# Performance work log

Measured on AMD Instinct MI355X. Metric: run time of the kernel, lower is better.

The kernel has to match this reference:

```python
import jax, jax.numpy as jnp
import numpy as np

B, N, T, D, H, K = 8, 100, 16, 4, 64, 2
E = N * (N - 1)  # 9900 directed edges (fully connected, no self-loops)


def setup_inputs() -> dict:
    key = jax.random.key(0)
    ks = jax.random.split(key, 12)
    inputs = jax.random.normal(ks[0], (B, N, T, D), jnp.float32)
    # edge-type distribution per directed pair (softmax over K types)
    rel_type = jax.nn.softmax(jax.random.normal(ks[1], (B, E, K), jnp.float32), axis=-1)
    # one-hot receiver / sender incidence matrices for fully-connected graph
    off = ~np.eye(N, dtype=bool)
    send_idx, rec_idx = np.where(off)
    eye = np.eye(N, dtype=np.float32)
    rel_rec = jnp.asarray(eye[rec_idx])    # [E, N]
    rel_send = jnp.asarray(eye[send_idx])  # [E, N]
    s = 0.1
    msg_fc1_w = jax.random.normal(ks[2], (K, H, 2 * D), jnp.float32) * s
    msg_fc1_b = jax.random.normal(ks[3], (K, H), jnp.float32) * s
    msg_fc2_w = jax.random.normal(ks[4], (K, H, H), jnp.float32) * s
    msg_fc2_b = jax.random.normal(ks[5], (K, H), jnp.float32) * s
    out_fc1_w = jax.random.normal(ks[6], (H, D + H), jnp.float32) * s
    out_fc1_b = jax.random.normal(ks[7], (H,), jnp.float32) * s
    out_fc2_w = jax.random.normal(ks[8], (H, H), jnp.float32) * s
    out_fc2_b = jax.random.normal(ks[9], (H,), jnp.float32) * s
    out_fc3_w = jax.random.normal(ks[10], (D, H), jnp.float32) * s
    out_fc3_b = jax.random.normal(ks[11], (D,), jnp.float32) * s
    return {
        "inputs": inputs, "rel_type": rel_type,
        "rel_rec": rel_rec, "rel_send": rel_send,
        "msg_fc1_w": msg_fc1_w, "msg_fc1_b": msg_fc1_b,
        "msg_fc2_w": msg_fc2_w, "msg_fc2_b": msg_fc2_b,
        "out_fc1_w": out_fc1_w, "out_fc1_b": out_fc1_b,
        "out_fc2_w": out_fc2_w, "out_fc2_b": out_fc2_b,
        "out_fc3_w": out_fc3_w, "out_fc3_b": out_fc3_b,
        "pred_steps": 1,
    }


def reference(inputs, rel_type, rel_rec, rel_send,
              msg_fc1_w, msg_fc1_b, msg_fc2_w, msg_fc2_b,
              out_fc1_w, out_fc1_b, out_fc2_w, out_fc2_b,
              out_fc3_w, out_fc3_b, pred_steps):
    # inputs: [B, N, T, D] -> [B, T, N, D]
    x = jnp.transpose(inputs, (0, 2, 1, 3))
    b, t, n, d = x.shape
    # rel_type: [B, E, K] -> [B, T, E, K]
    rt = jnp.broadcast_to(rel_type[:, None], (b, t, rel_type.shape[1], rel_type.shape[2]))

    def single_step(xs, rts):
        # gather endpoint states: [B, T', E, D]
        recv = jnp.einsum('en,btnd->bted', rel_rec, xs)
        send = jnp.einsum('en,btnd->bted', rel_send, xs)
        pre_msg = jnp.concatenate([send, recv], axis=-1)  # [B, T', E, 2D]
        # per-edge-type MLP, skipping edge type 0 (skip_first_edge_type=True)
        h1 = jax.nn.relu(jnp.einsum('btef,khf->btekh', pre_msg, msg_fc1_w[1:]) + msg_fc1_b[1:])
        h2 = jax.nn.relu(jnp.einsum('btekh,kgh->btekg', h1, msg_fc2_w[1:]) + msg_fc2_b[1:])
        # mask by edge-type weight and sum over types -> [B, T', E, H]
        all_msgs = jnp.einsum('btekh,btek->bteh', h2, rts[..., 1:])
        # aggregate messages at receivers: [B, T', N, H]
        agg = jnp.einsum('bteh,en->btnh', all_msgs, rel_rec)
        aug = jnp.concatenate([xs, agg], axis=-1)  # [B, T', N, D+H]
        p = jax.nn.relu(aug @ out_fc1_w.T + out_fc1_b)
        p = jax.nn.relu(p @ out_fc2_w.T + out_fc2_b)
        p = p @ out_fc3_w.T + out_fc3_b
        return xs + p

    last_pred = x[:, 0::pred_steps]
    curr_rt = rt[:, 0::pred_steps]
    preds = []
    for _ in range(pred_steps):
        last_pred = single_step(last_pred, curr_rt)
        preds.append(last_pred)
    tp = preds[0].shape[1]
    # interleave: output[:, i::pred_steps] = preds[i]
    output = jnp.stack(preds, axis=2).reshape(b, tp * pred_steps, n, d)
    pred_all = output[:, : t - 1]  # [B, T-1, N, D]
    return jnp.transpose(pred_all, (0, 2, 1, 3))  # [B, N, T-1, D]
```

## Files before the change

### kernel.cpp

```cpp
#include <hip/hip_runtime.h>
#include <hip/hip_fp16.h>

#define B_  8
#define N_  100
#define T_  16
#define TP_ 15
#define D_  4
#define H_  64
#define E_  9900
#define NG  25
#define ROWS 12000

#define WS_AIN 0u
#define WS_V   2304000u
#define WS_RTT 3840000u
#define WS_UBF 4198400u
#define WS_W2F 5928960u
#define WS_W1F 5937152u
#define WS_W2B 5949440u
#define WS_W3F 5957632u

typedef __attribute__((ext_vector_type(8))) _Float16 f16x8;
typedef __attribute__((ext_vector_type(4))) float f32x4;

__device__ __forceinline__ void gload_lds16(const void* g, void* lds) {
    __builtin_amdgcn_global_load_lds(
        (const __attribute__((address_space(1))) void*)g,
        (__attribute__((address_space(3))) void*)lds, 16, 0, 0);
}

__device__ __forceinline__ f16x8 relu_add8(uint4 u, uint4 v) {
    const f16x8 a = __builtin_bit_cast(f16x8, u);
    const f16x8 b = __builtin_bit_cast(f16x8, v);
    const f16x8 s = a + b;
    const f16x8 z = (f16x8)(_Float16)0;
    return __builtin_elementwise_max(s, z);
}

__global__ __launch_bounds__(256)
void nri_prep(const float* __restrict__ x, const float* __restrict__ rel,
              const float* __restrict__ w1, const float* __restrict__ b1,
              const float* __restrict__ w2, const float* __restrict__ f1w,
              const float* __restrict__ f2w, const float* __restrict__ f3w,
              __half* __restrict__ ubf, __half* __restrict__ v_h,
              float* __restrict__ rtt, __half* __restrict__ ain,
              __half* __restrict__ w2f, __half* __restrict__ w1f,
              __half* __restrict__ w2b, __half* __restrict__ w3f)
{
    const int lane = threadIdx.x & 63;
    const int wid  = blockIdx.x * 4 + (threadIdx.x >> 6);

    if (wid < ROWS) {
        const int nn = wid % N_;
        const int bt = wid / N_;
        const int t  = bt % TP_;
        const int b  = bt / TP_;
        const float4 ws4 = *(const float4*)(w1 + lane * 8);
        const float4 wr4 = *(const float4*)(w1 + lane * 8 + 4);
        const float4 xv  = *(const float4*)(x + (((size_t)b * N_ + nn) * T_ + t) * D_);
        const float u = ws4.x * xv.x + ws4.y * xv.y + ws4.z * xv.z + ws4.w * xv.w;
        const float v = wr4.x * xv.x + wr4.y * xv.y + wr4.z * xv.z + wr4.w * xv.w
                        + b1[lane];
        ubf[(size_t)bt * 7200 + nn * 72 + lane] = __float2half(u);
        v_h[(size_t)wid * 64 + lane] = __float2half(v);
        if (lane == 32) {
            const unsigned short h0 = __half_as_ushort(__float2half(xv.x));
            const unsigned short h1 = __half_as_ushort(__float2half(xv.y));
            const unsigned short h2 = __half_as_ushort(__float2half(xv.z));
            const unsigned short h3 = __half_as_ushort(__float2half(xv.w));
            uint2 p; p.x = (unsigned)h0 | ((unsigned)h1 << 16);
                     p.y = (unsigned)h2 | ((unsigned)h3 << 16);
            *(uint2*)(ain + (size_t)wid * 96 + 64) = p;
        } else if (lane >= 33 && lane < 40) {
            uint2 zz; zz.x = 0u; zz.y = 0u;
            *(uint2*)(ain + (size_t)wid * 96 + 68 + (lane - 33) * 4) = zz;
        }
    } else if (wid < ROWS + B_ * N_) {
        const int idx = wid - ROWS;
        const int n = idx % N_;
        const int b = idx / N_;
        float* dst = rtt + (size_t)idx * 112;
        const int ia  = lane + (lane >= n ? 1 : 0);
        const int eda = ia * (N_ - 1) + (n < ia ? n : n - 1);
        dst[lane] = rel[((size_t)b * E_ + eda) * 2 + 1];
        if (lane < 48) {
            const int e2 = 64 + lane;
            float rv = 0.f;
            if (e2 < N_ - 1) {
                const int ib  = e2 + (e2 >= n ? 1 : 0);
                const int edb = ib * (N_ - 1) + (n < ib ? n : n - 1);
                rv = rel[((size_t)b * E_ + edb) * 2 + 1];
            }
            dst[64 + lane] = rv;
        }
    } else {
        const int fid = wid - (ROWS + B_ * N_);
        const int g16 = lane & 15, q = lane >> 4;
        unsigned short h[8];
        if (fid < 8) {
            const int s = fid >> 2, nt = fid & 3;
            const int g = nt * 16 + g16;
            #pragma unroll
            for (int j = 0; j < 8; ++j)
                h[j] = __half_as_ushort(__float2half(
                    w2[(size_t)g * 64 + s * 32 + q * 8 + j]));
            uint4 pv; pv.x = h[0] | ((unsigned)h[1] << 16); pv.y = h[2] | ((unsigned)h[3] << 16);
                      pv.z = h[4] | ((unsigned)h[5] << 16); pv.w = h[6] | ((unsigned)h[7] << 16);
            *(uint4*)(w2f + fid * 512 + lane * 8) = pv;
        } else if (fid < 20) {
            const int f = fid - 8;
            const int s = f >> 2, nt = f & 3;
            const int g = nt * 16 + g16;
            #pragma unroll
            for (int j = 0; j < 8; ++j) {
                const int k = s * 32 + q * 8 + j;
                float v = 0.f;
                if (k < 64)       v = f1w[(size_t)g * 68 + 4 + k];
                else if (k < 68)  v = f1w[(size_t)g * 68 + (k - 64)];
                h[j] = __half_as_ushort(__float2half(v));
            }
            uint4 pv; pv.x = h[0] | ((unsigned)h[1] << 16); pv.y = h[2] | ((unsigned)h[3] << 16);
                      pv.z = h[4] | ((unsigned)h[5] << 16); pv.w = h[6] | ((unsigned)h[7] << 16);
            *(uint4*)(w1f + f * 512 + lane * 8) = pv;
        } else if (fid < 28) {
            const int f = fid - 20;
            const int s = f >> 2, nt = f & 3;
            const int g = nt * 16 + g16;
            #pragma unroll
            for (int j = 0; j < 8; ++j)
                h[j] = __half_as_ushort(__float2half(
                    f2w[(size_t)g * 64 + s * 32 + q * 8 + j]));
            uint4 pv; pv.x = h[0] | ((unsigned)h[1] << 16); pv.y = h[2] | ((unsigned)h[3] << 16);
                      pv.z = h[4] | ((unsigned)h[5] << 16); pv.w = h[6] | ((unsigned)h[7] << 16);
            *(uint4*)(w2b + f * 512 + lane * 8) = pv;
        } else if (fid == 28) {
            unsigned short hh[16];
            #pragma unroll
            for (int nt = 0; nt < 4; ++nt)
                #pragma unroll
                for (int d = 0; d < 4; ++d)
                    hh[nt * 4 + d] = __half_as_ushort(__float2half(
                        f3w[d * 64 + nt * 16 + g16]));
            uint4 p0, p1;
            p0.x = hh[0] | ((unsigned)hh[1] << 16);  p0.y = hh[2] | ((unsigned)hh[3] << 16);
            p0.z = hh[4] | ((unsigned)hh[5] << 16);  p0.w = hh[6] | ((unsigned)hh[7] << 16);
            p1.x = hh[8] | ((unsigned)hh[9] << 16);  p1.y = hh[10] | ((unsigned)hh[11] << 16);
            p1.z = hh[12] | ((unsigned)hh[13] << 16); p1.w = hh[14] | ((unsigned)hh[15] << 16);
            *(uint4*)(w3f + lane * 16) = p0;
            *(uint4*)(w3f + lane * 16 + 8) = p1;
        }
    }
}

__global__ __launch_bounds__(256)
void nri_agg(const __half* __restrict__ ubf, const __half* __restrict__ v_h,
             const float* __restrict__ rtt, const __half* __restrict__ w2f,
             const float* __restrict__ b2, __half* __restrict__ ain)
{
    __shared__ __half u_lds[7680];

    const int tid  = threadIdx.x;
    const int lane = tid & 63;
    const int w    = tid >> 6;
    const int bid  = blockIdx.x;
    const int g  = bid % NG;
    const int t  = (bid / NG) % TP_;
    const int b  = bid / (NG * TP_);
    const int bt = b * TP_ + t;

    {
        const char* gsrc = (const char*)(ubf + (size_t)bt * 7200);
        char* ldst = (char*)u_lds;
        #pragma unroll
        for (int j = 0; j < 4; ++j) {
            const int c = w + 4 * j;
            if (c < 15)
                gload_lds16(gsrc + c * 1024 + lane * 16, ldst + c * 1024);
        }
    }

    const int col = lane & 15;
    const int q   = lane >> 4;
    const int kq  = q * 8;

    f16x8 bfr[8];
    #pragma unroll
    for (int f = 0; f < 8; ++f)
        bfr[f] = *(const f16x8*)((const char*)w2f + f * 1024 + lane * 16);

    const int n   = g * 4 + w;
    const int row = bt * N_ + n;
    const __half* vp = v_h + (size_t)row * 64;
    const uint4 vv0 = *(const uint4*)(vp + kq);
    const uint4 vv1 = *(const uint4*)(vp + 32 + kq);
    float bb[4];
    #pragma unroll
    for (int nt = 0; nt < 4; ++nt) bb[nt] = b2[nt * 16 + col];
    const float* rtp = rtt + ((size_t)b * N_ + n) * 112 + q * 4;

    __syncthreads();

    float aggl[4] = {0.f, 0.f, 0.f, 0.f};
    #pragma unroll
    for (int mf = 0; mf < 7; ++mf) {
        const int e = mf * 16 + col;
        int i = e + (e >= n ? 1 : 0);
        if (i > N_ - 1) i = N_ - 1;
        const float4 rt4 = *(const float4*)(rtp + mf * 16);
        f32x4 acc[4] = {};
        const uint4 ud0 = *(const uint4*)&u_lds[i * 72 + kq];
        const f16x8 af0 = relu_add8(ud0, vv0);
        #pragma unroll
        for (int nt = 0; nt < 4; ++nt)
            acc[nt] = __builtin_amdgcn_mfma_f32_16x16x32_f16(af0, bfr[nt], acc[nt], 0, 0, 0);
        const uint4 ud1 = *(const uint4*)&u_lds[i * 72 + 32 + kq];
        const f16x8 af1 = relu_add8(ud1, vv1);
        #pragma unroll
        for (int nt = 0; nt < 4; ++nt)
            acc[nt] = __builtin_amdgcn_mfma_f32_16x16x32_f16(af1, bfr[4 + nt], acc[nt], 0, 0, 0);
        #pragma unroll
        for (int nt = 0; nt < 4; ++nt) {
            aggl[nt] += fmaxf(acc[nt][0] + bb[nt], 0.f) * rt4.x
                      + fmaxf(acc[nt][1] + bb[nt], 0.f) * rt4.y
                      + fmaxf(acc[nt][2] + bb[nt], 0.f) * rt4.z
                      + fmaxf(acc[nt][3] + bb[nt], 0.f) * rt4.w;
        }
    }
    #pragma unroll
    for (int nt = 0; nt < 4; ++nt) {
        float p = aggl[nt];
        p += __shfl_xor(p, 16, 64);
        p += __shfl_xor(p, 32, 64);
        if (lane < 16)
            ain[(size_t)row * 96 + nt * 16 + col] = __float2half(p);
    }
}

__global__ __launch_bounds__(256)
void nri_out(const __half* __restrict__ ain, const __half* __restrict__ w1f,
             const __half* __restrict__ w2b, const __half* __restrict__ w3f,
             const float* __restrict__ f1b, const float* __restrict__ f2b,
             const float* __restrict__ f3b, const float* __restrict__ x,
             float* __restrict__ out)
{
    __shared__ __half p1buf[4][16 * 72];

    const int tid  = threadIdx.x;
    const int lane = tid & 63;
    const int w    = tid >> 6;
    const int row0 = (blockIdx.x * 4 + w) * 16;
    if (row0 >= ROWS) return;

    const int col = lane & 15;
    const int q   = lane >> 4;
    const int kq  = q * 8;

    f16x8 w1r[12];
    #pragma unroll
    for (int f = 0; f < 12; ++f)
        w1r[f] = *(const f16x8*)((const char*)w1f + f * 1024 + lane * 16);
    f16x8 w2r[8];
    #pragma unroll
    for (int f = 0; f < 8; ++f)
        w2r[f] = *(const f16x8*)((const char*)w2b + f * 1024 + lane * 16);
    float b1v[4], b2v[4];
    #pragma unroll
    for (int nt = 0; nt < 4; ++nt) { b1v[nt] = f1b[nt * 16 + col]; b2v[nt] = f2b[nt * 16 + col]; }
    const float4 b3v = *(const float4*)f3b;
    float w3v[16];
    {
        const uint4 p0 = *(const uint4*)(w3f + col * 16);
        const uint4 p1 = *(const uint4*)(w3f + col * 16 + 8);
        const unsigned* pp0 = (const unsigned*)&p0;
        const unsigned* pp1 = (const unsigned*)&p1;
        #pragma unroll
        for (int i = 0; i < 4; ++i) {
            w3v[2*i]     = __half2float(__ushort_as_half((unsigned short)(pp0[i] & 0xffff)));
            w3v[2*i + 1] = __half2float(__ushort_as_half((unsigned short)(pp0[i] >> 16)));
            w3v[8 + 2*i]     = __half2float(__ushort_as_half((unsigned short)(pp1[i] & 0xffff)));
            w3v[8 + 2*i + 1] = __half2float(__ushort_as_half((unsigned short)(pp1[i] >> 16)));
        }
    }

    f32x4 acc1[4] = {};
    #pragma unroll
    for (int s = 0; s < 3; ++s) {
        const uint4 ad = *(const uint4*)(ain + (size_t)(row0 + col) * 96 + s * 32 + kq);
        const f16x8 af = __builtin_bit_cast(f16x8, ad);
        #pragma unroll
        for (int nt = 0; nt < 4; ++nt)
            acc1[nt] = __builtin_amdgcn_mfma_f32_16x16x32_f16(af, w1r[s * 4 + nt], acc1[nt], 0, 0, 0);
    }
    #pragma unroll
    for (int nt = 0; nt < 4; ++nt)
        #pragma unroll
        for (int j = 0; j < 4; ++j)
            p1buf[w][(q * 4 + j) * 72 + nt * 16 + col] =
                __float2half(fmaxf(acc1[nt][j] + b1v[nt], 0.f));
    asm volatile("s_waitcnt lgkmcnt(0)" ::: "memory");
    __builtin_amdgcn_wave_barrier();

    f32x4 acc2[4] = {};
    #pragma unroll
    for (int s = 0; s < 2; ++s) {
        const uint4 pd = *(const uint4*)&p1buf[w][col * 72 + s * 32 + kq];
        const f16x8 af = __builtin_bit_cast(f16x8, pd);
        #pragma unroll
        for (int nt = 0; nt < 4; ++nt)
            acc2[nt] = __builtin_amdgcn_mfma_f32_16x16x32_f16(af, w2r[s * 4 + nt], acc2[nt], 0, 0, 0);
    }
    float p2v[4][4];
    #pragma unroll
    for (int nt = 0; nt < 4; ++nt)
        #pragma unroll
        for (int j = 0; j < 4; ++j)
            p2v[nt][j] = fmaxf(acc2[nt][j] + b2v[nt], 0.f);

    float pr[4][4];
    #pragma unroll
    for (int d = 0; d < 4; ++d)
        #pragma unroll
        for (int j = 0; j < 4; ++j) {
            float s = w3v[0 * 4 + d] * p2v[0][j] + w3v[1 * 4 + d] * p2v[1][j]
                    + w3v[2 * 4 + d] * p2v[2][j] + w3v[3 * 4 + d] * p2v[3][j];
            s += __shfl_xor(s, 1, 64);
            s += __shfl_xor(s, 2, 64);
            s += __shfl_xor(s, 4, 64);
            s += __shfl_xor(s, 8, 64);
            pr[d][j] = s;
        }

    if (col == 0) {
        #pragma unroll
        for (int j = 0; j < 4; ++j) {
            const int rg = row0 + q * 4 + j;
            const int n  = rg % N_;
            const int bt = rg / N_;
            const int t  = bt % TP_;
            const int b  = bt / TP_;
            const float4 xv = *(const float4*)(x + (((size_t)b * N_ + n) * T_ + t) * D_);
            float4 o;
            o.x = xv.x + b3v.x + pr[0][j];
            o.y = xv.y + b3v.y + pr[1][j];
            o.z = xv.z + b3v.z + pr[2][j];
            o.w = xv.w + b3v.w + pr[3][j];
            *(float4*)(out + (((size_t)b * N_ + n) * TP_ + t) * D_) = o;
        }
    }
}

extern "C" void kernel_launch(void* const* d_in, const int* in_sizes, int n_in,
                              void* d_out, int out_size, void* d_ws, size_t ws_size,
                              hipStream_t stream) {
    const float* x   = (const float*)d_in[0];
    const float* rel = (const float*)d_in[1];
    const float* w1  = (const float*)d_in[4] + 1 * H_ * 2 * D_;
    const float* b1  = (const float*)d_in[5] + 1 * H_;
    const float* w2  = (const float*)d_in[6] + 1 * H_ * H_;
    const float* b2  = (const float*)d_in[7] + 1 * H_;
    const float* f1w = (const float*)d_in[8];
    const float* f1b = (const float*)d_in[9];
    const float* f2w = (const float*)d_in[10];
    const float* f2b = (const float*)d_in[11];
    const float* f3w = (const float*)d_in[12];
    const float* f3b = (const float*)d_in[13];
    float* out = (float*)d_out;

    unsigned char* ws = (unsigned char*)d_ws;
    __half* ain = (__half*)(ws + WS_AIN);
    __half* v_h = (__half*)(ws + WS_V);
    float*  rtt = (float*)(ws + WS_RTT);
    __half* ubf = (__half*)(ws + WS_UBF);
    __half* w2f = (__half*)(ws + WS_W2F);
    __half* w1f = (__half*)(ws + WS_W1F);
    __half* w2b = (__half*)(ws + WS_W2B);
    __half* w3f = (__half*)(ws + WS_W3F);

    nri_prep<<<dim3(3208), 256, 0, stream>>>(x, rel, w1, b1, w2, f1w, f2w, f3w,
                                             ubf, v_h, rtt, ain,
                                             w2f, w1f, w2b, w3f);
    nri_agg<<<dim3(B_ * TP_ * NG), 256, 0, stream>>>(ubf, v_h, rtt, w2f, b2, ain);
    nri_out<<<dim3((ROWS / 16 + 3) / 4), 256, 0, stream>>>(ain, w1f, w2b, w3f,
                                                           f1b, f2b, f3b, x, out);
}
```

Measured before the change: 39.57 us.

## Fuse aggregation and output MLP into one kernel with LDS-resident intermediates

Merges the nri_agg and nri_out kernels into a single nri_main kernel. Each block now handles 16 receiver nodes of one (b,t) instead of 4, so the aggregated rows and the x features stay in LDS and are fed straight into the output MLP. The receiver-side projection v is computed on the fly from x instead of being written to global memory by the prep kernel. This removes one launch and the global round trips for ain and v_h. In exchange, the grid shrinks from 3000 to 840 blocks, each wave serially loops over 4 nodes, and only one wave does the output MLP, so parallelism and occupancy drop.

Measured after the change: 40.83 us. 3.2% more time.

```diff
diff --git a/kernel.cpp b/kernel.cpp
--- a/kernel.cpp
+++ b/kernel.cpp
@@ -8,17 +8,15 @@
 #define D_  4
 #define H_  64
 #define E_  9900
-#define NG  25
+#define NG2 7
 #define ROWS 12000
 
-#define WS_AIN 0u
-#define WS_V   2304000u
-#define WS_RTT 3840000u
-#define WS_UBF 4198400u
-#define WS_W2F 5928960u
-#define WS_W1F 5937152u
-#define WS_W2B 5949440u
-#define WS_W3F 5957632u
+#define WS_RTT 0u
+#define WS_UBF 358400u
+#define WS_W2F 2088960u
+#define WS_W1F 2097152u
+#define WS_W2B 2109440u
+#define WS_W3F 2117632u
 
 typedef __attribute__((ext_vector_type(8))) _Float16 f16x8;
 typedef __attribute__((ext_vector_type(4))) float f32x4;
@@ -39,11 +37,10 @@
 
 __global__ __launch_bounds__(256)
 void nri_prep(const float* __restrict__ x, const float* __restrict__ rel,
-              const float* __restrict__ w1, const float* __restrict__ b1,
-              const float* __restrict__ w2, const float* __restrict__ f1w,
-              const float* __restrict__ f2w, const float* __restrict__ f3w,
-              __half* __restrict__ ubf, __half* __restrict__ v_h,
-              float* __restrict__ rtt, __half* __restrict__ ain,
+              const float* __restrict__ w1, const float* __restrict__ w2,
+              const float* __restrict__ f1w, const float* __restrict__ f2w,
+              const float* __restrict__ f3w,
+              __half* __restrict__ ubf, float* __restrict__ rtt,
               __half* __restrict__ w2f, __half* __restrict__ w1f,
               __half* __restrict__ w2b, __half* __restrict__ w3f)
 {
@@ -56,25 +53,9 @@
         const int t  = bt % TP_;
         const int b  = bt / TP_;
         const float4 ws4 = *(const float4*)(w1 + lane * 8);
-        const float4 wr4 = *(const float4*)(w1 + lane * 8 + 4);
         const float4 xv  = *(const float4*)(x + (((size_t)b * N_ + nn) * T_ + t) * D_);
-        const float u = ws4.x * xv.x + ws4.y * xv.y + ws4.z * xv.z + ws4.w * xv.w;
-        const float v = wr4.x * xv.x + wr4.y * xv.y + wr4.z * xv.z + wr4.w * xv.w
-                        + b1[lane];
-        ubf[(size_t)bt * 7200 + nn * 72 + lane] = __float2half(u);
-        v_h[(size_t)wid * 64 + lane] = __float2half(v);
-        if (lane == 32) {
-            const unsigned short h0 = __half_as_ushort(__float2half(xv.x));
-            const unsigned short h1 = __half_as_ushort(__float2half(xv.y));
-            const unsigned short h2 = __half_as_ushort(__float2half(xv.z));
-            const unsigned short h3 = __half_as_ushort(__float2half(xv.w));
-            uint2 p; p.x = (unsigned)h0 | ((unsigned)h1 << 16);
-                     p.y = (unsigned)h2 | ((unsigned)h3 << 16);
-            *(uint2*)(ain + (size_t)wid * 96 + 64) = p;
-        } else if (lane >= 33 && lane < 40) {
-            uint2 zz; zz.x = 0u; zz.y = 0u;
-            *(uint2*)(ain + (size_t)wid * 96 + 68 + (lane - 33) * 4) = zz;
-        }
+        ubf[(size_t)bt * 7200 + nn * 72 + lane] =
+            __float2half(ws4.x * xv.x + ws4.y * xv.y + ws4.z * xv.z + ws4.w * xv.w);
     } else if (wid < ROWS + B_ * N_) {
         const int idx = wid - ROWS;
         const int n = idx % N_;
@@ -153,19 +134,27 @@
 }
 
 __global__ __launch_bounds__(256)
-void nri_agg(const __half* __restrict__ ubf, const __half* __restrict__ v_h,
-             const float* __restrict__ rtt, const __half* __restrict__ w2f,
-             const float* __restrict__ b2, __half* __restrict__ ain)
+void nri_main(const __half* __restrict__ ubf, const float* __restrict__ rtt,
+              const __half* __restrict__ w2f, const float* __restrict__ b2,
+              const float* __restrict__ w1, const float* __restrict__ b1,
+              const __half* __restrict__ w1f, const __half* __restrict__ w2b,
+              const __half* __restrict__ w3f,
+              const float* __restrict__ f1b, const float* __restrict__ f2b,
+              const float* __restrict__ f3b,
+              const float* __restrict__ x, float* __restrict__ out)
 {
     __shared__ __half u_lds[7680];
+    __shared__ __half ain[16][104];
+    __shared__ __half v_lds[4][72];
+    __shared__ __half p1buf[16][72];
 
     const int tid  = threadIdx.x;
     const int lane = tid & 63;
     const int w    = tid >> 6;
     const int bid  = blockIdx.x;
-    const int g  = bid % NG;
-    const int t  = (bid / NG) % TP_;
-    const int b  = bid / (NG * TP_);
+    const int g  = bid % NG2;
+    const int t  = (bid / NG2) % TP_;
+    const int b  = bid / (NG2 * TP_);
     const int bt = b * TP_ + t;
 
     {
@@ -183,90 +172,137 @@
     const int q   = lane >> 4;
     const int kq  = q * 8;
 
+    if (tid < 224) {
+        const int r = tid / 14, u = tid % 14;
+        *(unsigned*)&ain[r][68 + u * 2] = 0u;
+    }
+
+    const float4 wr4 = *(const float4*)(w1 + lane * 8 + 4);
+    const float  bv1 = b1[lane];
+
     f16x8 bfr[8];
     #pragma unroll
     for (int f = 0; f < 8; ++f)
         bfr[f] = *(const f16x8*)((const char*)w2f + f * 1024 + lane * 16);
-
-    const int n   = g * 4 + w;
-    const int row = bt * N_ + n;
-    const __half* vp = v_h + (size_t)row * 64;
-    const uint4 vv0 = *(const uint4*)(vp + kq);
-    const uint4 vv1 = *(const uint4*)(vp + 32 + kq);
     float bb[4];
     #pragma unroll
     for (int nt = 0; nt < 4; ++nt) bb[nt] = b2[nt * 16 + col];
-    const float* rtp = rtt + ((size_t)b * N_ + n) * 112 + q * 4;
 
     __syncthreads();
 
-    float aggl[4] = {0.f, 0.f, 0.f, 0.f};
-    #pragma unroll
-    for (int mf = 0; mf < 7; ++mf) {
-        const int e = mf * 16 + col;
-        int i = e + (e >= n ? 1 : 0);
-        if (i > N_ - 1) i = N_ - 1;
-        const float4 rt4 = *(const float4*)(rtp + mf * 16);
-        f32x4 acc[4] = {};
-        const uint4 ud0 = *(const uint4*)&u_lds[i * 72 + kq];
-        const f16x8 af0 = relu_add8(ud0, vv0);
-        #pragma unroll
-        for (int nt = 0; nt < 4; ++nt)
-            acc[nt] = __builtin_amdgcn_mfma_f32_16x16x32_f16(af0, bfr[nt], acc[nt], 0, 0, 0);
-        const uint4 ud1 = *(const uint4*)&u_lds[i * 72 + 32 + kq];
-        const f16x8 af1 = relu_add8(ud1, vv1);
-        #pragma unroll
-        for (int nt = 0; nt < 4; ++nt)
-            acc[nt] = __builtin_amdgcn_mfma_f32_16x16x32_f16(af1, bfr[4 + nt], acc[nt], 0, 0, 0);
-        #pragma unroll
-        for (int nt = 0; nt < 4; ++nt) {
-            aggl[nt] += fmaxf(acc[nt][0] + bb[nt], 0.f) * rt4.x
-                      + fmaxf(acc[nt][1] + bb[nt], 0.f) * rt4.y
-                      + fmaxf(acc[nt][2] + bb[nt], 0.f) * rt4.z
-                      + fmaxf(acc[nt][3] + bb[nt], 0.f) * rt4.w;
-        }
-    }
-    #pragma unroll
-    for (int nt = 0; nt < 4; ++nt) {
-        float p = aggl[nt];
-        p += __shfl_xor(p, 16, 64);
-        p += __shfl_xor(p, 32, 64);
-        if (lane < 16)
-            ain[(size_t)row * 96 + nt * 16 + col] = __float2half(p);
-    }
-}
-
-__global__ __launch_bounds__(256)
-void nri_out(const __half* __restrict__ ain, const __half* __restrict__ w1f,
-             const __half* __restrict__ w2b, const __half* __restrict__ w3f,
-             const float* __restrict__ f1b, const float* __restrict__ f2b,
-             const float* __restrict__ f3b, const float* __restrict__ x,
-             float* __restrict__ out)
-{
-    __shared__ __half p1buf[4][16 * 72];
-
-    const int tid  = threadIdx.x;
-    const int lane = tid & 63;
-    const int w    = tid >> 6;
-    const int row0 = (blockIdx.x * 4 + w) * 16;
-    if (row0 >= ROWS) return;
-
-    const int col = lane & 15;
-    const int q   = lane >> 4;
-    const int kq  = q * 8;
+    #pragma unroll 1
+    for (int r = 0; r < 4; ++r) {
+        const int n = g * 16 + r * 4 + w;
+        if (n < N_) {
+            const int row = r * 4 + w;
+            const float4 xr = *(const float4*)(
+                x + (((size_t)b * N_ + n) * T_ + t) * D_);
+            v_lds[w][lane] = __float2half(
+                wr4.x * xr.x + wr4.y * xr.y + wr4.z * xr.z + wr4.w * xr.w + bv1);
+            if (lane < 4) {
+                const float xc = (lane == 0) ? xr.x : (lane == 1) ? xr.y
+                               : (lane == 2) ? xr.z : xr.w;
+                ain[row][64 + lane] = __float2half(xc);
+            }
+            __builtin_amdgcn_wave_barrier();
+            const uint4 vv0 = *(const uint4*)&v_lds[w][kq];
+            const uint4 vv1 = *(const uint4*)&v_lds[w][32 + kq];
+            const float* rtp = rtt + ((size_t)b * N_ + n) * 112 + q * 4;
+
+            float aggl[4] = {0.f, 0.f, 0.f, 0.f};
+            #pragma unroll
+            for (int mf = 0; mf < 7; ++mf) {
+                const int e = mf * 16 + col;
+                int i = e + (e >= n ? 1 : 0);
+                if (i > N_ - 1) i = N_ - 1;
+                const float4 rt4 = *(const float4*)(rtp + mf * 16);
+                f32x4 acc[4] = {};
+                const uint4 ud0 = *(const uint4*)&u_lds[i * 72 + kq];
+                f16x8 af = relu_add8(ud0, vv0);
+                #pragma unroll
+                for (int nt = 0; nt < 4; ++nt)
+                    acc[nt] = __builtin_amdgcn_mfma_f32_16x16x32_f16(
+                        af, bfr[nt], acc[nt], 0, 0, 0);
+                const uint4 ud1 = *(const uint4*)&u_lds[i * 72 + 32 + kq];
+                af = relu_add8(ud1, vv1);
+                #pragma unroll
+                for (int nt = 0; nt < 4; ++nt)
+                    acc[nt] = __builtin_amdgcn_mfma_f32_16x16x32_f16(
+                        af, bfr[4 + nt], acc[nt], 0, 0, 0);
+                #pragma unroll
+                for (int nt = 0; nt < 4; ++nt) {
+                    aggl[nt] += fmaxf(acc[nt][0] + bb[nt], 0.f) * rt4.x
+                              + fmaxf(acc[nt][1] + bb[nt], 0.f) * rt4.y
+                              + fmaxf(acc[nt][2] + bb[nt], 0.f) * rt4.z
+                              + fmaxf(acc[nt][3] + bb[nt], 0.f) * rt4.w;
+                }
+            }
+            #pragma unroll
+            for (int nt = 0; nt < 4; ++nt) {
+                float p = aggl[nt];
+                p += __shfl_xor(p, 16, 64);
+                p += __shfl_xor(p, 32, 64);
+                if (lane < 16)
+                    ain[row][nt * 16 + col] = __float2half(p);
+            }
+        }
+    }
+    __syncthreads();
+
+    if (w != 0) return;
 
     f16x8 w1r[12];
     #pragma unroll
     for (int f = 0; f < 12; ++f)
         w1r[f] = *(const f16x8*)((const char*)w1f + f * 1024 + lane * 16);
+    float b1v[4];
+    #pragma unroll
+    for (int nt = 0; nt < 4; ++nt) b1v[nt] = f1b[nt * 16 + col];
+
+    f32x4 acc1[4] = {};
+    #pragma unroll
+    for (int s = 0; s < 3; ++s) {
+        const uint4 ad = *(const uint4*)&ain[col][s * 32 + kq];
+        const f16x8 af = __builtin_bit_cast(f16x8, ad);
+        #pragma unroll
+        for (int nt = 0; nt < 4; ++nt)
+            acc1[nt] = __builtin_amdgcn_mfma_f32_16x16x32_f16(
+                af, w1r[s * 4 + nt], acc1[nt], 0, 0, 0);
+    }
+    #pragma unroll
+    for (int nt = 0; nt < 4; ++nt)
+        #pragma unroll
+        for (int j = 0; j < 4; ++j)
+            p1buf[q * 4 + j][nt * 16 + col] =
+                __float2half(fmaxf(acc1[nt][j] + b1v[nt], 0.f));
+    asm volatile("s_waitcnt lgkmcnt(0)" ::: "memory");
+    __builtin_amdgcn_wave_barrier();
+
     f16x8 w2r[8];
     #pragma unroll
     for (int f = 0; f < 8; ++f)
         w2r[f] = *(const f16x8*)((const char*)w2b + f * 1024 + lane * 16);
-    float b1v[4], b2v[4];
-    #pragma unroll
-    for (int nt = 0; nt < 4; ++nt) { b1v[nt] = f1b[nt * 16 + col]; b2v[nt] = f2b[nt * 16 + col]; }
-    const float4 b3v = *(const float4*)f3b;
+    float b2v[4];
+    #pragma unroll
+    for (int nt = 0; nt < 4; ++nt) b2v[nt] = f2b[nt * 16 + col];
+
+    f32x4 acc2[4] = {};
+    #pragma unroll
+    for (int s = 0; s < 2; ++s) {
+        const uint4 pd = *(const uint4*)&p1buf[col][s * 32 + kq];
+        const f16x8 af = __builtin_bit_cast(f16x8, pd);
+        #pragma unroll
+        for (int nt = 0; nt < 4; ++nt)
+            acc2[nt] = __builtin_amdgcn_mfma_f32_16x16x32_f16(
+                af, w2r[s * 4 + nt], acc2[nt], 0, 0, 0);
+    }
+    float p2v[4][4];
+    #pragma unroll
+    for (int nt = 0; nt < 4; ++nt)
+        #pragma unroll
+        for (int j = 0; j < 4; ++j)
+            p2v[nt][j] = fmaxf(acc2[nt][j] + b2v[nt], 0.f);
+
     float w3v[16];
     {
         const uint4 p0 = *(const uint4*)(w3f + col * 16);
@@ -281,41 +317,7 @@
             w3v[8 + 2*i + 1] = __half2float(__ushort_as_half((unsigned short)(pp1[i] >> 16)));
         }
     }
-
-    f32x4 acc1[4] = {};
-    #pragma unroll
-    for (int s = 0; s < 3; ++s) {
-        const uint4 ad = *(const uint4*)(ain + (size_t)(row0 + col) * 96 + s * 32 + kq);
-        const f16x8 af = __builtin_bit_cast(f16x8, ad);
-        #pragma unroll
-        for (int nt = 0; nt < 4; ++nt)
-            acc1[nt] = __builtin_amdgcn_mfma_f32_16x16x32_f16(af, w1r[s * 4 + nt], acc1[nt], 0, 0, 0);
-    }
-    #pragma unroll
-    for (int nt = 0; nt < 4; ++nt)
-        #pragma unroll
-        for (int j = 0; j < 4; ++j)
-            p1buf[w][(q * 4 + j) * 72 + nt * 16 + col] =
-                __float2half(fmaxf(acc1[nt][j] + b1v[nt], 0.f));
-    asm volatile("s_waitcnt lgkmcnt(0)" ::: "memory");
-    __builtin_amdgcn_wave_barrier();
-
-    f32x4 acc2[4] = {};
-    #pragma unroll
-    for (int s = 0; s < 2; ++s) {
-        const uint4 pd = *(const uint4*)&p1buf[w][col * 72 + s * 32 + kq];
-        const f16x8 af = __builtin_bit_cast(f16x8, pd);
-        #pragma unroll
-        for (int nt = 0; nt < 4; ++nt)
-            acc2[nt] = __builtin_amdgcn_mfma_f32_16x16x32_f16(af, w2r[s * 4 + nt], acc2[nt], 0, 0, 0);
-    }
-    float p2v[4][4];
-    #pragma unroll
-    for (int nt = 0; nt < 4; ++nt)
-        #pragma unroll
-        for (int j = 0; j < 4; ++j)
-            p2v[nt][j] = fmaxf(acc2[nt][j] + b2v[nt], 0.f);
-
+    const float4 b3v = *(const float4*)f3b;
     float pr[4][4];
     #pragma unroll
     for (int d = 0; d < 4; ++d)
@@ -333,18 +335,18 @@
     if (col == 0) {
         #pragma unroll
         for (int j = 0; j < 4; ++j) {
-            const int rg = row0 + q * 4 + j;
-            const int n  = rg % N_;
-            const int bt = rg / N_;
-            const int t  = bt % TP_;
-            const int b  = bt / TP_;
-            const float4 xv = *(const float4*)(x + (((size_t)b * N_ + n) * T_ + t) * D_);
-            float4 o;
-            o.x = xv.x + b3v.x + pr[0][j];
-            o.y = xv.y + b3v.y + pr[1][j];
-            o.z = xv.z + b3v.z + pr[2][j];
-            o.w = xv.w + b3v.w + pr[3][j];
-            *(float4*)(out + (((size_t)b * N_ + n) * TP_ + t) * D_) = o;
+            const int rr = q * 4 + j;
+            const int n  = g * 16 + rr;
+            if (n < N_) {
+                const float4 xv = *(const float4*)(
+                    x + (((size_t)b * N_ + n) * T_ + t) * D_);
+                float4 o;
+                o.x = xv.x + b3v.x + pr[0][j];
+                o.y = xv.y + b3v.y + pr[1][j];
+                o.z = xv.z + b3v.z + pr[2][j];
+                o.w = xv.w + b3v.w + pr[3][j];
+                *(float4*)(out + (((size_t)b * N_ + n) * TP_ + t) * D_) = o;
+            }
         }
     }
 }
@@ -367,8 +369,6 @@
     float* out = (float*)d_out;
 
     unsigned char* ws = (unsigned char*)d_ws;
-    __half* ain = (__half*)(ws + WS_AIN);
-    __half* v_h = (__half*)(ws + WS_V);
     float*  rtt = (float*)(ws + WS_RTT);
     __half* ubf = (__half*)(ws + WS_UBF);
     __half* w2f = (__half*)(ws + WS_W2F);
@@ -376,10 +376,8 @@
     __half* w2b = (__half*)(ws + WS_W2B);
     __half* w3f = (__half*)(ws + WS_W3F);
 
-    nri_prep<<<dim3(3208), 256, 0, stream>>>(x, rel, w1, b1, w2, f1w, f2w, f3w,
-                                             ubf, v_h, rtt, ain,
-                                             w2f, w1f, w2b, w3f);
-    nri_agg<<<dim3(B_ * TP_ * NG), 256, 0, stream>>>(ubf, v_h, rtt, w2f, b2, ain);
-    nri_out<<<dim3((ROWS / 16 + 3) / 4), 256, 0, stream>>>(ain, w1f, w2b, w3f,
-                                                           f1b, f2b, f3b, x, out);
-}
+    nri_prep<<<dim3(3208), 256, 0, stream>>>(x, rel, w1, w2, f1w, f2w, f3w,
+                                             ubf, rtt, w2f, w1f, w2b, w3f);
+    nri_main<<<dim3(B_ * TP_ * NG2), 256, 0, stream>>>(
+        ubf, rtt, w2f, b2, w1, b1, w1f, w2b, w3f, f1b, f2b, f3b, x, out);
+}
```

## Split agg edge loop across two wave halves and use single-wave out blocks

Applied to the files above, without the earlier changes.

nri_agg now launches 512 threads per block, and two waves share each node: one covers edge fragments 0-3, the other 4-6. Their partial sums are reduced through shared memory before the store. This shortens the serial MFMA chain per wave and raises wave-level parallelism, at the cost of an extra barrier and duplicated weight-register loads. nri_out becomes one wave per block, 64 threads each, to spread rows across more CUs; it also drops the explicit lgkmcnt wait before the wave barrier, which may risk an LDS ordering hazard.

Result: slower. 49.11 us (+24.1%).

```diff
diff --git a/kernel.cpp b/kernel.cpp
--- a/kernel.cpp
+++ b/kernel.cpp
@@ -152,16 +152,19 @@
     }
 }
 
-__global__ __launch_bounds__(256)
+__global__ __launch_bounds__(512)
 void nri_agg(const __half* __restrict__ ubf, const __half* __restrict__ v_h,
              const float* __restrict__ rtt, const __half* __restrict__ w2f,
              const float* __restrict__ b2, __half* __restrict__ ain)
 {
     __shared__ __half u_lds[7680];
+    __shared__ float part[8][64];
 
     const int tid  = threadIdx.x;
     const int lane = tid & 63;
     const int w    = tid >> 6;
+    const int half = w >> 2;
+    const int wr   = w & 3;
     const int bid  = blockIdx.x;
     const int g  = bid % NG;
     const int t  = (bid / NG) % TP_;
@@ -172,8 +175,8 @@
         const char* gsrc = (const char*)(ubf + (size_t)bt * 7200);
         char* ldst = (char*)u_lds;
         #pragma unroll
-        for (int j = 0; j < 4; ++j) {
-            const int c = w + 4 * j;
+        for (int j = 0; j < 2; ++j) {
+            const int c = w + 8 * j;
             if (c < 15)
                 gload_lds16(gsrc + c * 1024 + lane * 16, ldst + c * 1024);
         }
@@ -188,7 +191,7 @@
     for (int f = 0; f < 8; ++f)
         bfr[f] = *(const f16x8*)((const char*)w2f + f * 1024 + lane * 16);
 
-    const int n   = g * 4 + w;
+    const int n   = g * 4 + wr;
     const int row = bt * N_ + n;
     const __half* vp = v_h + (size_t)row * 64;
     const uint4 vv0 = *(const uint4*)(vp + kq);
@@ -201,23 +204,22 @@
     __syncthreads();
 
     float aggl[4] = {0.f, 0.f, 0.f, 0.f};
-    #pragma unroll
-    for (int mf = 0; mf < 7; ++mf) {
+    auto do_mf = [&](int mf) {
         const int e = mf * 16 + col;
         int i = e + (e >= n ? 1 : 0);
         if (i > N_ - 1) i = N_ - 1;
         const float4 rt4 = *(const float4*)(rtp + mf * 16);
         f32x4 acc[4] = {};
         const uint4 ud0 = *(const uint4*)&u_lds[i * 72 + kq];
-        const f16x8 af0 = relu_add8(ud0, vv0);
+        f16x8 af = relu_add8(ud0, vv0);
         #pragma unroll
         for (int nt = 0; nt < 4; ++nt)
-            acc[nt] = __builtin_amdgcn_mfma_f32_16x16x32_f16(af0, bfr[nt], acc[nt], 0, 0, 0);
+            acc[nt] = __builtin_amdgcn_mfma_f32_16x16x32_f16(af, bfr[nt], acc[nt], 0, 0, 0);
         const uint4 ud1 = *(const uint4*)&u_lds[i * 72 + 32 + kq];
-        const f16x8 af1 = relu_add8(ud1, vv1);
+        af = relu_add8(ud1, vv1);
         #pragma unroll
         for (int nt = 0; nt < 4; ++nt)
-            acc[nt] = __builtin_amdgcn_mfma_f32_16x16x32_f16(af1, bfr[4 + nt], acc[nt], 0, 0, 0);
+            acc[nt] = __builtin_amdgcn_mfma_f32_16x16x32_f16(af, bfr[4 + nt], acc[nt], 0, 0, 0);
         #pragma unroll
         for (int nt = 0; nt < 4; ++nt) {
             aggl[nt] += fmaxf(acc[nt][0] + bb[nt], 0.f) * rt4.x
@@ -225,31 +227,45 @@
                       + fmaxf(acc[nt][2] + bb[nt], 0.f) * rt4.z
                       + fmaxf(acc[nt][3] + bb[nt], 0.f) * rt4.w;
         }
-    }
+    };
+    if (half == 0) {
+        #pragma unroll
+        for (int mf = 0; mf < 4; ++mf) do_mf(mf);
+    } else {
+        #pragma unroll
+        for (int mf = 4; mf < 7; ++mf) do_mf(mf);
+    }
+
     #pragma unroll
     for (int nt = 0; nt < 4; ++nt) {
         float p = aggl[nt];
         p += __shfl_xor(p, 16, 64);
         p += __shfl_xor(p, 32, 64);
-        if (lane < 16)
-            ain[(size_t)row * 96 + nt * 16 + col] = __float2half(p);
-    }
-}
-
-__global__ __launch_bounds__(256)
+        if (lane < 16) part[w][nt * 16 + col] = p;
+    }
+    __syncthreads();
+
+    if (half == 0 && lane < 16) {
+        #pragma unroll
+        for (int nt = 0; nt < 4; ++nt) {
+            const int gg = nt * 16 + col;
+            ain[(size_t)row * 96 + gg] =
+                __float2half(part[w][gg] + part[w + 4][gg]);
+        }
+    }
+}
+
+__global__ __launch_bounds__(64)
 void nri_out(const __half* __restrict__ ain, const __half* __restrict__ w1f,
              const __half* __restrict__ w2b, const __half* __restrict__ w3f,
              const float* __restrict__ f1b, const float* __restrict__ f2b,
              const float* __restrict__ f3b, const float* __restrict__ x,
              float* __restrict__ out)
 {
-    __shared__ __half p1buf[4][16 * 72];
-
-    const int tid  = threadIdx.x;
-    const int lane = tid & 63;
-    const int w    = tid >> 6;
-    const int row0 = (blockIdx.x * 4 + w) * 16;
-    if (row0 >= ROWS) return;
+    __shared__ __half p1buf[16 * 72];
+
+    const int lane = threadIdx.x & 63;
+    const int row0 = blockIdx.x * 16;
 
     const int col = lane & 15;
     const int q   = lane >> 4;
@@ -295,15 +311,14 @@
     for (int nt = 0; nt < 4; ++nt)
         #pragma unroll
         for (int j = 0; j < 4; ++j)
-            p1buf[w][(q * 4 + j) * 72 + nt * 16 + col] =
+            p1buf[(q * 4 + j) * 72 + nt * 16 + col] =
                 __float2half(fmaxf(acc1[nt][j] + b1v[nt], 0.f));
-    asm volatile("s_waitcnt lgkmcnt(0)" ::: "memory");
     __builtin_amdgcn_wave_barrier();
 
     f32x4 acc2[4] = {};
     #pragma unroll
     for (int s = 0; s < 2; ++s) {
-        const uint4 pd = *(const uint4*)&p1buf[w][col * 72 + s * 32 + kq];
+        const uint4 pd = *(const uint4*)&p1buf[col * 72 + s * 32 + kq];
         const f16x8 af = __builtin_bit_cast(f16x8, pd);
         #pragma unroll
         for (int nt = 0; nt < 4; ++nt)
@@ -379,7 +394,7 @@
     nri_prep<<<dim3(3208), 256, 0, stream>>>(x, rel, w1, b1, w2, f1w, f2w, f3w,
                                              ubf, v_h, rtt, ain,
                                              w2f, w1f, w2b, w3f);
-    nri_agg<<<dim3(B_ * TP_ * NG), 256, 0, stream>>>(ubf, v_h, rtt, w2f, b2, ain);
-    nri_out<<<dim3((ROWS / 16 + 3) / 4), 256, 0, stream>>>(ain, w1f, w2b, w3f,
-                                                           f1b, f2b, f3b, x, out);
-}
+    nri_agg<<<dim3(B_ * TP_ * NG), 512, 0, stream>>>(ubf, v_h, rtt, w2f, b2, ain);
+    nri_out<<<dim3(ROWS / 16), 64, 0, stream>>>(ain, w1f, w2b, w3f,
+                                                f1b, f2b, f3b, x, out);
+}
```

## Fuse first message-layer projection into aggregation kernel, dropping u/v workspace buffers

Applied to the files above, without the earlier changes.

Moves the per-node sender/receiver projections from the prep kernel into the aggregation kernel. Each block now computes the u rows for its (b,t) directly into LDS and its own v row, so the ubf and v_h global buffers and their round-trip traffic are gone, and the prep grid shrinks. It also seeds the MFMA accumulators with the bias and uses fmaf for the weighted sum. The cost is that the projection is recomputed 25 times per (b,t), once by each block sharing it, and the aggregation kernel now also writes the input features and padding into ain.

Result: slower. 42.78 us (+8.1%).

```diff
diff --git a/kernel.cpp b/kernel.cpp
--- a/kernel.cpp
+++ b/kernel.cpp
@@ -12,22 +12,14 @@
 #define ROWS 12000
 
 #define WS_AIN 0u
-#define WS_V   2304000u
-#define WS_RTT 3840000u
-#define WS_UBF 4198400u
-#define WS_W2F 5928960u
-#define WS_W1F 5937152u
-#define WS_W2B 5949440u
-#define WS_W3F 5957632u
+#define WS_RTT 2304000u
+#define WS_W2F 2662400u
+#define WS_W1F 2670592u
+#define WS_W2B 2682880u
+#define WS_W3F 2691072u
 
 typedef __attribute__((ext_vector_type(8))) _Float16 f16x8;
 typedef __attribute__((ext_vector_type(4))) float f32x4;
-
-__device__ __forceinline__ void gload_lds16(const void* g, void* lds) {
-    __builtin_amdgcn_global_load_lds(
-        (const __attribute__((address_space(1))) void*)g,
-        (__attribute__((address_space(3))) void*)lds, 16, 0, 0);
-}
 
 __device__ __forceinline__ f16x8 relu_add8(uint4 u, uint4 v) {
     const f16x8 a = __builtin_bit_cast(f16x8, u);
@@ -38,48 +30,20 @@
 }
 
 __global__ __launch_bounds__(256)
-void nri_prep(const float* __restrict__ x, const float* __restrict__ rel,
-              const float* __restrict__ w1, const float* __restrict__ b1,
+void nri_prep(const float* __restrict__ rel,
               const float* __restrict__ w2, const float* __restrict__ f1w,
               const float* __restrict__ f2w, const float* __restrict__ f3w,
-              __half* __restrict__ ubf, __half* __restrict__ v_h,
-              float* __restrict__ rtt, __half* __restrict__ ain,
+              float* __restrict__ rtt,
               __half* __restrict__ w2f, __half* __restrict__ w1f,
               __half* __restrict__ w2b, __half* __restrict__ w3f)
 {
     const int lane = threadIdx.x & 63;
     const int wid  = blockIdx.x * 4 + (threadIdx.x >> 6);
 
-    if (wid < ROWS) {
-        const int nn = wid % N_;
-        const int bt = wid / N_;
-        const int t  = bt % TP_;
-        const int b  = bt / TP_;
-        const float4 ws4 = *(const float4*)(w1 + lane * 8);
-        const float4 wr4 = *(const float4*)(w1 + lane * 8 + 4);
-        const float4 xv  = *(const float4*)(x + (((size_t)b * N_ + nn) * T_ + t) * D_);
-        const float u = ws4.x * xv.x + ws4.y * xv.y + ws4.z * xv.z + ws4.w * xv.w;
-        const float v = wr4.x * xv.x + wr4.y * xv.y + wr4.z * xv.z + wr4.w * xv.w
-                        + b1[lane];
-        ubf[(size_t)bt * 7200 + nn * 72 + lane] = __float2half(u);
-        v_h[(size_t)wid * 64 + lane] = __float2half(v);
-        if (lane == 32) {
-            const unsigned short h0 = __half_as_ushort(__float2half(xv.x));
-            const unsigned short h1 = __half_as_ushort(__float2half(xv.y));
-            const unsigned short h2 = __half_as_ushort(__float2half(xv.z));
-            const unsigned short h3 = __half_as_ushort(__float2half(xv.w));
-            uint2 p; p.x = (unsigned)h0 | ((unsigned)h1 << 16);
-                     p.y = (unsigned)h2 | ((unsigned)h3 << 16);
-            *(uint2*)(ain + (size_t)wid * 96 + 64) = p;
-        } else if (lane >= 33 && lane < 40) {
-            uint2 zz; zz.x = 0u; zz.y = 0u;
-            *(uint2*)(ain + (size_t)wid * 96 + 68 + (lane - 33) * 4) = zz;
-        }
-    } else if (wid < ROWS + B_ * N_) {
-        const int idx = wid - ROWS;
-        const int n = idx % N_;
-        const int b = idx / N_;
-        float* dst = rtt + (size_t)idx * 112;
+    if (wid < B_ * N_) {
+        const int n = wid % N_;
+        const int b = wid / N_;
+        float* dst = rtt + (size_t)wid * 112;
         const int ia  = lane + (lane >= n ? 1 : 0);
         const int eda = ia * (N_ - 1) + (n < ia ? n : n - 1);
         dst[lane] = rel[((size_t)b * E_ + eda) * 2 + 1];
@@ -94,7 +58,7 @@
             dst[64 + lane] = rv;
         }
     } else {
-        const int fid = wid - (ROWS + B_ * N_);
+        const int fid = wid - B_ * N_;
         const int g16 = lane & 15, q = lane >> 4;
         unsigned short h[8];
         if (fid < 8) {
@@ -153,11 +117,13 @@
 }
 
 __global__ __launch_bounds__(256)
-void nri_agg(const __half* __restrict__ ubf, const __half* __restrict__ v_h,
-             const float* __restrict__ rtt, const __half* __restrict__ w2f,
-             const float* __restrict__ b2, __half* __restrict__ ain)
+void nri_agg(const float* __restrict__ x, const float* __restrict__ w1,
+             const float* __restrict__ b1, const float* __restrict__ rtt,
+             const __half* __restrict__ w2f, const float* __restrict__ b2,
+             __half* __restrict__ ain)
 {
-    __shared__ __half u_lds[7680];
+    __shared__ __half u_lds[N_ * 72];
+    __shared__ __half v_lds[4][72];
 
     const int tid  = threadIdx.x;
     const int lane = tid & 63;
@@ -168,31 +134,36 @@
     const int b  = bid / (NG * TP_);
     const int bt = b * TP_ + t;
 
-    {
-        const char* gsrc = (const char*)(ubf + (size_t)bt * 7200);
-        char* ldst = (char*)u_lds;
-        #pragma unroll
-        for (int j = 0; j < 4; ++j) {
-            const int c = w + 4 * j;
-            if (c < 15)
-                gload_lds16(gsrc + c * 1024 + lane * 16, ldst + c * 1024);
-        }
-    }
-
     const int col = lane & 15;
     const int q   = lane >> 4;
     const int kq  = q * 8;
 
+    const float4 ws4 = *(const float4*)(w1 + lane * 8);
+    const float4 wr4 = *(const float4*)(w1 + lane * 8 + 4);
+
+    #pragma unroll
+    for (int it = 0; it < 25; ++it) {
+        const int r = it * 4 + w;
+        const float4 xv = *(const float4*)(
+            x + (((size_t)b * N_ + r) * T_ + t) * D_);
+        u_lds[r * 72 + lane] = __float2half(
+            ws4.x * xv.x + ws4.y * xv.y + ws4.z * xv.z + ws4.w * xv.w);
+    }
+
+    const int n   = g * 4 + w;
+    const int row = bt * N_ + n;
+    const float4 xr = *(const float4*)(
+        x + (((size_t)b * N_ + n) * T_ + t) * D_);
+    v_lds[w][lane] = __float2half(
+        wr4.x * xr.x + wr4.y * xr.y + wr4.z * xr.z + wr4.w * xr.w + b1[lane]);
+    __builtin_amdgcn_wave_barrier();
+    const uint4 vv0 = *(const uint4*)&v_lds[w][kq];
+    const uint4 vv1 = *(const uint4*)&v_lds[w][32 + kq];
+
     f16x8 bfr[8];
     #pragma unroll
     for (int f = 0; f < 8; ++f)
         bfr[f] = *(const f16x8*)((const char*)w2f + f * 1024 + lane * 16);
-
-    const int n   = g * 4 + w;
-    const int row = bt * N_ + n;
-    const __half* vp = v_h + (size_t)row * 64;
-    const uint4 vv0 = *(const uint4*)(vp + kq);
-    const uint4 vv1 = *(const uint4*)(vp + 32 + kq);
     float bb[4];
     #pragma unroll
     for (int nt = 0; nt < 4; ++nt) bb[nt] = b2[nt * 16 + col];
@@ -207,23 +178,28 @@
         int i = e + (e >= n ? 1 : 0);
         if (i > N_ - 1) i = N_ - 1;
         const float4 rt4 = *(const float4*)(rtp + mf * 16);
-        f32x4 acc[4] = {};
+        f32x4 acc[4];
+        #pragma unroll
+        for (int nt = 0; nt < 4; ++nt) {
+            acc[nt][0] = bb[nt]; acc[nt][1] = bb[nt];
+            acc[nt][2] = bb[nt]; acc[nt][3] = bb[nt];
+        }
         const uint4 ud0 = *(const uint4*)&u_lds[i * 72 + kq];
-        const f16x8 af0 = relu_add8(ud0, vv0);
+        f16x8 af = relu_add8(ud0, vv0);
         #pragma unroll
         for (int nt = 0; nt < 4; ++nt)
-            acc[nt] = __builtin_amdgcn_mfma_f32_16x16x32_f16(af0, bfr[nt], acc[nt], 0, 0, 0);
+            acc[nt] = __builtin_amdgcn_mfma_f32_16x16x32_f16(af, bfr[nt], acc[nt], 0, 0, 0);
         const uint4 ud1 = *(const uint4*)&u_lds[i * 72 + 32 + kq];
-        const f16x8 af1 = relu_add8(ud1, vv1);
+        af = relu_add8(ud1, vv1);
         #pragma unroll
         for (int nt = 0; nt < 4; ++nt)
-            acc[nt] = __builtin_amdgcn_mfma_f32_16x16x32_f16(af1, bfr[4 + nt], acc[nt], 0, 0, 0);
+            acc[nt] = __builtin_amdgcn_mfma_f32_16x16x32_f16(af, bfr[4 + nt], acc[nt], 0, 0, 0);
         #pragma unroll
         for (int nt = 0; nt < 4; ++nt) {
-            aggl[nt] += fmaxf(acc[nt][0] + bb[nt], 0.f) * rt4.x
-                      + fmaxf(acc[nt][1] + bb[nt], 0.f) * rt4.y
-                      + fmaxf(acc[nt][2] + bb[nt], 0.f) * rt4.z
-                      + fmaxf(acc[nt][3] + bb[nt], 0.f) * rt4.w;
+            aggl[nt] = fmaf(fmaxf(acc[nt][0], 0.f), rt4.x, aggl[nt]);
+            aggl[nt] = fmaf(fmaxf(acc[nt][1], 0.f), rt4.y, aggl[nt]);
+            aggl[nt] = fmaf(fmaxf(acc[nt][2], 0.f), rt4.z, aggl[nt]);
+            aggl[nt] = fmaf(fmaxf(acc[nt][3], 0.f), rt4.w, aggl[nt]);
         }
     }
     #pragma unroll
@@ -233,6 +209,13 @@
         p += __shfl_xor(p, 32, 64);
         if (lane < 16)
             ain[(size_t)row * 96 + nt * 16 + col] = __float2half(p);
+    }
+    if (lane >= 32 && lane < 36) {
+        const float xc = (lane == 32) ? xr.x : (lane == 33) ? xr.y
+                       : (lane == 34) ? xr.z : xr.w;
+        ain[(size_t)row * 96 + 64 + (lane - 32)] = __float2half(xc);
+    } else if (lane >= 36 && lane < 50) {
+        *(unsigned*)(ain + (size_t)row * 96 + 68 + (lane - 36) * 2) = 0u;
     }
 }
 
@@ -368,18 +351,15 @@
 
     unsigned char* ws = (unsigned char*)d_ws;
     __half* ain = (__half*)(ws + WS_AIN);
-    __half* v_h = (__half*)(ws + WS_V);
     float*  rtt = (float*)(ws + WS_RTT);
-    __half* ubf = (__half*)(ws + WS_UBF);
     __half* w2f = (__half*)(ws + WS_W2F);
     __half* w1f = (__half*)(ws + WS_W1F);
     __half* w2b = (__half*)(ws + WS_W2B);
     __half* w3f = (__half*)(ws + WS_W3F);
 
-    nri_prep<<<dim3(3208), 256, 0, stream>>>(x, rel, w1, b1, w2, f1w, f2w, f3w,
-                                             ubf, v_h, rtt, ain,
-                                             w2f, w1f, w2b, w3f);
-    nri_agg<<<dim3(B_ * TP_ * NG), 256, 0, stream>>>(ubf, v_h, rtt, w2f, b2, ain);
+    nri_prep<<<dim3(208), 256, 0, stream>>>(rel, w2, f1w, f2w, f3w,
+                                            rtt, w2f, w1f, w2b, w3f);
+    nri_agg<<<dim3(B_ * TP_ * NG), 256, 0, stream>>>(x, w1, b1, rtt, w2f, b2, ain);
     nri_out<<<dim3((ROWS / 16 + 3) / 4), 256, 0, stream>>>(ain, w1f, w2b, w3f,
                                                            f1b, f2b, f3b, x, out);
 }
```
